# Performance work log

Hardware: AMD Instinct MI355X
Metric: run time of the kernel (lower is better)

Reference implementation:

```python
import jax, jax.numpy as jnp
import numpy as np

D = 1024
HEADS = 16
HD = D // HEADS


def setup_inputs() -> dict:
    key = jax.random.key(0)
    kx, kqkv, kout = jax.random.split(key, 3)
    x = jax.random.normal(kx, (2, 2048, D), dtype=jnp.float32)
    # torch Linear weight is [out, in]; store same layout
    W_qkv = jax.random.normal(kqkv, (3 * D, D), dtype=jnp.float32) * (D ** -0.5)
    W_out = jax.random.normal(kout, (D, D), dtype=jnp.float32) * (D ** -0.5)
    return {"x": x, "W_qkv": W_qkv, "W_out": W_out}


def reference(x, W_qkv, W_out):
    B, T, _ = x.shape
    scale = HD ** -0.5
    qkv = jnp.einsum('btd,ed->bte', x, W_qkv)            # [B,T,3D]
    qkv = qkv.reshape(B, T, 3, HEADS, HD)
    q = jnp.transpose(qkv[:, :, 0], (0, 2, 1, 3))        # [B,H,T,hd]
    k = jnp.transpose(qkv[:, :, 1], (0, 2, 1, 3))
    v = jnp.transpose(qkv[:, :, 2], (0, 2, 1, 3))
    attn = jnp.einsum('bhqd,bhkd->bhqk', q, k) * scale   # [B,H,T,T]
    causal = jnp.tril(jnp.ones((T, T), dtype=bool))
    attn = jnp.where(causal, attn, -jnp.inf)
    attn = jax.nn.softmax(attn, axis=-1)
    out = jnp.einsum('bhqk,bhkd->bhqd', attn, v)         # [B,H,T,hd]
    out = jnp.transpose(out, (0, 2, 1, 3)).reshape(B, T, HEADS * HD)
    return jnp.einsum('btd,ed->bte', out, W_out)
```

## Files before the change

kernel.cpp:

```cpp
#include <hip/hip_runtime.h>
#include <cmath>


typedef unsigned short u16;
typedef unsigned int u32;
typedef short short8 __attribute__((ext_vector_type(8)));
typedef float floatx4 __attribute__((ext_vector_type(4)));

#define T_SZ 2048
#define HD_SZ 64
#define LOG2E 1.44269504088896f

__device__ __forceinline__ u16 f2bf(float f) {
  unsigned u = __float_as_uint(f);
  u += 0x7fffu + ((u >> 16) & 1u);
  return (u16)(u >> 16);
}

__device__ __forceinline__ u32 pack_bf2(float lo, float hi) {
  return __builtin_amdgcn_perm(__float_as_uint(hi), __float_as_uint(lo), 0x07060302u);
}

__device__ __forceinline__ void gload16(const u16* g, u16* l) {
  __builtin_amdgcn_global_load_lds(
      (const __attribute__((address_space(1))) void*)g,
      (__attribute__((address_space(3))) void*)l, 16, 0, 0);
}

__global__ __launch_bounds__(256) void cast3(const float* __restrict__ a, u16* __restrict__ ao, int na4,
                                             const float* __restrict__ b, u16* __restrict__ bo, int nb4,
                                             const float* __restrict__ c, u16* __restrict__ co, int nc4) {
  int i = blockIdx.x * 256 + threadIdx.x;
  const float* src;
  u16* dst;
  int j;
  if (i < na4) { src = a; dst = ao; j = i; }
  else if (i < na4 + nb4) { src = b; dst = bo; j = i - na4; }
  else { j = i - na4 - nb4; if (j >= nc4) return; src = c; dst = co; }
  float4 f = ((const float4*)src)[j];
  ushort4 o;
  o.x = f2bf(f.x); o.y = f2bf(f.y); o.z = f2bf(f.z); o.w = f2bf(f.w);
  ((ushort4*)dst)[j] = o;
}

template <int EPI>
__global__ __launch_bounds__(256) void gemm128(const u16* __restrict__ A,
                                               const u16* __restrict__ Bt,
                                               float* __restrict__ Cout,
                                               u16* __restrict__ Qf,
                                               u16* __restrict__ Kf,
                                               u16* __restrict__ Vf,
                                               int Kdim) {
  __shared__ u16 As[128 * 32];
  __shared__ u16 Bs[128 * 32];
  const int tid = threadIdx.x;
  const int lane = tid & 63;
  const int wave = tid >> 6;
  const int quad = lane >> 4;
  const int l16 = lane & 15;
  const int wm = wave >> 1, wn = wave & 1;
  const int m0 = blockIdx.y * 128;
  const int n0 = blockIdx.x * 128;

  floatx4 acc[4][4];
#pragma unroll
  for (int i = 0; i < 4; i++)
#pragma unroll
    for (int j = 0; j < 4; j++) acc[i][j] = (floatx4){0.f, 0.f, 0.f, 0.f};

  const int lrow = lane >> 2;
  const int pseg = lane & 3;
  const int lseg = pseg ^ ((lane >> 3) & 3);
  const u16* gsrc = (wave < 2) ? A : Bt;
  const int base_rc = (wave < 2) ? m0 : n0;
  u16* lbase = ((wave < 2) ? As : Bs) + ((wave & 1) * 64) * 32;
  const u16* gp[4];
  u16* lp[4];
#pragma unroll
  for (int j = 0; j < 4; j++) {
    const int row = (wave & 1) * 64 + j * 16 + lrow;
    gp[j] = gsrc + (size_t)(base_rc + row) * Kdim + lseg * 8;
    lp[j] = lbase + (j * 16) * 32 + lane * 8;
  }

  const int fsw = ((l16 >> 1) & 3);

  for (int k0 = 0; k0 < Kdim; k0 += 32) {
    __syncthreads();
#pragma unroll
    for (int j = 0; j < 4; j++) gload16(gp[j] + k0, lp[j]);
    __syncthreads();

    short8 af[4], bf[4];
#pragma unroll
    for (int mt = 0; mt < 4; mt++) {
      const int r = wm * 64 + mt * 16 + l16;
      af[mt] = *(const short8*)&As[r * 32 + (quad ^ fsw) * 8];
    }
#pragma unroll
    for (int nt = 0; nt < 4; nt++) {
      const int r = wn * 64 + nt * 16 + l16;
      bf[nt] = *(const short8*)&Bs[r * 32 + (quad ^ fsw) * 8];
    }
#pragma unroll
    for (int mt = 0; mt < 4; mt++)
#pragma unroll
      for (int nt = 0; nt < 4; nt++)
        acc[mt][nt] = __builtin_amdgcn_mfma_f32_16x16x32_bf16(af[mt], bf[nt], acc[mt][nt], 0, 0, 0);
  }

  if constexpr (EPI == 1) {
#pragma unroll
    for (int mt = 0; mt < 4; mt++)
#pragma unroll
      for (int nt = 0; nt < 4; nt++)
#pragma unroll
        for (int r = 0; r < 4; r++) {
          const int m = m0 + wm * 64 + mt * 16 + quad * 4 + r;
          const int n = n0 + wn * 64 + nt * 16 + l16;
          Cout[(size_t)m * 1024 + n] = acc[mt][nt][r];
        }
  } else {
    __shared__ u16 Ep[4][64 * 72];
    u16* ep = &Ep[wave][0];
    const int dest = n0 >> 10;
    const int n0w = n0 + wn * 64;
    const int m_abs = m0 + wm * 64;
    const int b = m_abs >> 11;
    const int t0w = m_abs & 2047;
    const int h = (n0w >> 6) & 15;
    const int bh = b * 16 + h;

    if (dest == 2) {
#pragma unroll
      for (int nt = 0; nt < 4; nt++) {
#pragma unroll
        for (int mt = 0; mt < 4; mt++) {
          uint2 w;
          w.x = pack_bf2(acc[mt][nt][0], acc[mt][nt][1]);
          w.y = pack_bf2(acc[mt][nt][2], acc[mt][nt][3]);
          *(uint2*)&ep[(nt * 16 + l16) * 72 + mt * 16 + quad * 4] = w;
        }
      }
    } else {
      const float sc = (dest == 0) ? 0.125f : 1.0f;
#pragma unroll
      for (int mt = 0; mt < 4; mt++)
#pragma unroll
        for (int nt = 0; nt < 4; nt++)
#pragma unroll
          for (int r = 0; r < 4; r++)
            ep[(mt * 16 + quad * 4 + r) * 72 + nt * 16 + l16] =
                f2bf(acc[mt][nt][r] * sc);
    }

    u16* dstp = (dest == 0) ? Qf : (dest == 1) ? Kf : Vf;
#pragma unroll
    for (int blk = 0; blk < 8; blk++) {
      const int tgd = blk >> 1;
      const int half = blk & 1;
      const int row = tgd * 16 + l16;
      const int col = half * 32 + quad * 8;
      const short8 v = *(const short8*)&ep[row * 72 + col];
      size_t base;
      if (dest == 0)
        base = ((size_t)(bh * 128 + (t0w >> 4) + tgd) * 2 + half) * 512;
      else
        base = (((size_t)(bh * 32 + (t0w >> 6)) * 4 + tgd) * 2 + half) * 512;
      *(short8*)(dstp + base + lane * 8) = v;
    }
  }
}

__global__ __launch_bounds__(256) void flash_attn(const u16* __restrict__ Qf,
                                                  const u16* __restrict__ Kf,
                                                  const u16* __restrict__ Vf,
                                                  u16* __restrict__ Og) {
  __shared__ u16 Ps[4][16 * 72];
  const int tid = threadIdx.x;
  const int lane = tid & 63, wave = tid >> 6;
  const int quad = lane >> 4, l16 = lane & 15;
  const int bh = blockIdx.x, p = blockIdx.y;
  const int b = bh >> 4, h = bh & 15;
  const u16* Qb = Qf + ((size_t)bh << 17);
  const u16* Kb = Kf + ((size_t)bh << 17);
  const u16* Vb = Vf + ((size_t)bh << 17);
  u16* ps = &Ps[wave][0];

  const int gs[2] = {p, 31 - p};

  for (int ph = 0; ph < 2; ph++) {
    const int g = gs[ph];
    const int t0 = g * 64 + wave * 16;
    const u16* qp = Qb + ((size_t)(g * 4 + wave)) * 1024 + lane * 8;
    const short8 qf0 = *(const short8*)qp;
    const short8 qf1 = *(const short8*)(qp + 512);

    float l_sum = 0.f;
    floatx4 o_acc[4];
#pragma unroll
    for (int dt = 0; dt < 4; dt++) o_acc[dt] = (floatx4){0.f, 0.f, 0.f, 0.f};

    for (int kt = 0; kt <= g; kt++) {
      const u16* kp = Kb + (size_t)kt * 4096 + lane * 8;
      const u16* vp = Vb + (size_t)kt * 4096 + lane * 8;
      const bool diag = (kt == g);

      short8 ka[4][2], va[4][2];
#pragma unroll
      for (int nt = 0; nt < 4; nt++) {
        ka[nt][0] = *(const short8*)(kp + (nt * 2 + 0) * 512);
        ka[nt][1] = *(const short8*)(kp + (nt * 2 + 1) * 512);
      }
#pragma unroll
      for (int dt = 0; dt < 4; dt++) {
        va[dt][0] = *(const short8*)(vp + (dt * 2 + 0) * 512);
        va[dt][1] = *(const short8*)(vp + (dt * 2 + 1) * 512);
      }

      floatx4 sacc[4];
#pragma unroll
      for (int nt = 0; nt < 4; nt++) {
        if (diag && nt > wave) continue;
        floatx4 s = (floatx4){0.f, 0.f, 0.f, 0.f};
        s = __builtin_amdgcn_mfma_f32_16x16x32_bf16(ka[nt][0], qf0, s, 0, 0, 0);
        s = __builtin_amdgcn_mfma_f32_16x16x32_bf16(ka[nt][1], qf1, s, 0, 0, 0);
        sacc[nt] = s;
      }

#pragma unroll
      for (int nt = 0; nt < 4; nt++) {
        float p0 = 0.f, p1 = 0.f, p2 = 0.f, p3 = 0.f;
        if (!(diag && nt > wave)) {
          p0 = exp2f(sacc[nt][0] * LOG2E);
          p1 = exp2f(sacc[nt][1] * LOG2E);
          p2 = exp2f(sacc[nt][2] * LOG2E);
          p3 = exp2f(sacc[nt][3] * LOG2E);
          if (diag && nt == wave) {
            if (quad * 4 + 0 > l16) p0 = 0.f;
            if (quad * 4 + 1 > l16) p1 = 0.f;
            if (quad * 4 + 2 > l16) p2 = 0.f;
            if (quad * 4 + 3 > l16) p3 = 0.f;
          }
          l_sum += (p0 + p1) + (p2 + p3);
        }
        uint2 w;
        w.x = pack_bf2(p0, p1);
        w.y = pack_bf2(p2, p3);
        *(uint2*)&ps[l16 * 72 + nt * 16 + quad * 4] = w;
      }

      const short8 pf0 = *(const short8*)&ps[l16 * 72 + quad * 8];
      const short8 pf1 = *(const short8*)&ps[l16 * 72 + 32 + quad * 8];

      const bool skip_hi = diag && (wave < 2);
#pragma unroll
      for (int dt = 0; dt < 4; dt++) {
        o_acc[dt] = __builtin_amdgcn_mfma_f32_16x16x32_bf16(va[dt][0], pf0, o_acc[dt], 0, 0, 0);
        if (!skip_hi)
          o_acc[dt] = __builtin_amdgcn_mfma_f32_16x16x32_bf16(va[dt][1], pf1, o_acc[dt], 0, 0, 0);
      }
    }

    l_sum += __shfl_xor(l_sum, 16, 64);
    l_sum += __shfl_xor(l_sum, 32, 64);
    const float inv_l = 1.0f / l_sum;

    const size_t row = ((size_t)(b * 2048 + t0 + l16) << 10) + h * 64;
#pragma unroll
    for (int dt = 0; dt < 4; dt++) {
      uint2 w;
      w.x = pack_bf2(o_acc[dt][0] * inv_l, o_acc[dt][1] * inv_l);
      w.y = pack_bf2(o_acc[dt][2] * inv_l, o_acc[dt][3] * inv_l);
      *(uint2*)&Og[row + dt * 16 + quad * 4] = w;
    }
  }
}

extern "C" void kernel_launch(void* const* d_in, const int* in_sizes, int n_in,
                              void* d_out, int out_size, void* d_ws, size_t ws_size,
                              hipStream_t stream) {
  const float* x = (const float*)d_in[0];
  const float* Wqkv = (const float*)d_in[1];
  const float* Wout = (const float*)d_in[2];
  float* out = (float*)d_out;

  char* ws = (char*)d_ws;
  u16* xb    = (u16*)(ws + 0);
  u16* wqkvb = (u16*)(ws + 8388608);
  u16* woutb = (u16*)(ws + 14680064);
  u16* Qf    = (u16*)(ws + 16777216);
  u16* Kf    = (u16*)(ws + 25165824);
  u16* Vf    = (u16*)(ws + 33554432);
  u16* attn  = (u16*)(ws + 41943040);

  cast3<<<8192, 256, 0, stream>>>(x, xb, 1048576, Wqkv, wqkvb, 786432,
                                  Wout, woutb, 262144);

  gemm128<0><<<dim3(24, 32), 256, 0, stream>>>(xb, wqkvb, nullptr, Qf, Kf, Vf, 1024);

  flash_attn<<<dim3(32, 16), 256, 0, stream>>>(Qf, Kf, Vf, attn);

  gemm128<1><<<dim3(8, 32), 256, 0, stream>>>(attn, woutb, out, nullptr, nullptr, nullptr, 1024);
}
```

Before: 181.8 us.

## Share K/V loads across paired query tiles and retile output GEMM

Flash attention now processes both paired query tiles in a single K/V loop, loading each K/V tile once and interleaving two independent softmax/PV streams. The log2e factor is folded into the Q scale to drop a multiply per exponent. The output GEMM uses 64-row tiles for more blocks, and the QKV epilogue LDS is halved by staging wave pairs sequentially. This raises register pressure in attention and adds a barrier in the QKV epilogue.

```diff
diff --git a/kernel.cpp b/kernel.cpp
--- a/kernel.cpp
+++ b/kernel.cpp
@@ -9,7 +9,7 @@
 
 #define T_SZ 2048
 #define HD_SZ 64
-#define LOG2E 1.44269504088896f
+#define QSCALE 0.1803368801111244f
 
 __device__ __forceinline__ u16 f2bf(float f) {
   unsigned u = __float_as_uint(f);
@@ -43,16 +43,15 @@
   ((ushort4*)dst)[j] = o;
 }
 
-template <int EPI>
-__global__ __launch_bounds__(256) void gemm128(const u16* __restrict__ A,
-                                               const u16* __restrict__ Bt,
-                                               float* __restrict__ Cout,
-                                               u16* __restrict__ Qf,
-                                               u16* __restrict__ Kf,
-                                               u16* __restrict__ Vf,
-                                               int Kdim) {
+__global__ __launch_bounds__(256) void gemm_qkv(const u16* __restrict__ A,
+                                                const u16* __restrict__ Bt,
+                                                u16* __restrict__ Qf,
+                                                u16* __restrict__ Kf,
+                                                u16* __restrict__ Vf) {
   __shared__ u16 As[128 * 32];
   __shared__ u16 Bs[128 * 32];
+  __shared__ u16 Ep[2][64 * 72];
+  const int Kdim = 1024;
   const int tid = threadIdx.x;
   const int lane = tid & 63;
   const int wave = tid >> 6;
@@ -109,41 +108,29 @@
         acc[mt][nt] = __builtin_amdgcn_mfma_f32_16x16x32_bf16(af[mt], bf[nt], acc[mt][nt], 0, 0, 0);
   }
 
-  if constexpr (EPI == 1) {
-#pragma unroll
-    for (int mt = 0; mt < 4; mt++)
-#pragma unroll
-      for (int nt = 0; nt < 4; nt++)
-#pragma unroll
-        for (int r = 0; r < 4; r++) {
-          const int m = m0 + wm * 64 + mt * 16 + quad * 4 + r;
-          const int n = n0 + wn * 64 + nt * 16 + l16;
-          Cout[(size_t)m * 1024 + n] = acc[mt][nt][r];
-        }
-  } else {
-    __shared__ u16 Ep[4][64 * 72];
-    u16* ep = &Ep[wave][0];
-    const int dest = n0 >> 10;
-    const int n0w = n0 + wn * 64;
-    const int m_abs = m0 + wm * 64;
-    const int b = m_abs >> 11;
-    const int t0w = m_abs & 2047;
-    const int h = (n0w >> 6) & 15;
-    const int bh = b * 16 + h;
-
+  const int dest = n0 >> 10;
+  const int n0w = n0 + wn * 64;
+  const int m_abs = m0 + wm * 64;
+  const int b = m_abs >> 11;
+  const int t0w = m_abs & 2047;
+  const int h = (n0w >> 6) & 15;
+  const int bh = b * 16 + h;
+  u16* dstp = (dest == 0) ? Qf : (dest == 1) ? Kf : Vf;
+
+  auto do_epi = [&](u16* ep) {
     if (dest == 2) {
 #pragma unroll
       for (int nt = 0; nt < 4; nt++) {
 #pragma unroll
         for (int mt = 0; mt < 4; mt++) {
           uint2 w;
-          w.x = pack_bf2(acc[mt][nt][0], acc[mt][nt][1]);
-          w.y = pack_bf2(acc[mt][nt][2], acc[mt][nt][3]);
+          w.x = (u32)f2bf(acc[mt][nt][0]) | ((u32)f2bf(acc[mt][nt][1]) << 16);
+          w.y = (u32)f2bf(acc[mt][nt][2]) | ((u32)f2bf(acc[mt][nt][3]) << 16);
           *(uint2*)&ep[(nt * 16 + l16) * 72 + mt * 16 + quad * 4] = w;
         }
       }
     } else {
-      const float sc = (dest == 0) ? 0.125f : 1.0f;
+      const float sc = (dest == 0) ? QSCALE : 1.0f;
 #pragma unroll
       for (int mt = 0; mt < 4; mt++)
 #pragma unroll
@@ -153,15 +140,11 @@
             ep[(mt * 16 + quad * 4 + r) * 72 + nt * 16 + l16] =
                 f2bf(acc[mt][nt][r] * sc);
     }
-
-    u16* dstp = (dest == 0) ? Qf : (dest == 1) ? Kf : Vf;
 #pragma unroll
     for (int blk = 0; blk < 8; blk++) {
       const int tgd = blk >> 1;
       const int half = blk & 1;
-      const int row = tgd * 16 + l16;
-      const int col = half * 32 + quad * 8;
-      const short8 v = *(const short8*)&ep[row * 72 + col];
+      const short8 v = *(const short8*)&ep[(tgd * 16 + l16) * 72 + half * 32 + quad * 8];
       size_t base;
       if (dest == 0)
         base = ((size_t)(bh * 128 + (t0w >> 4) + tgd) * 2 + half) * 512;
@@ -169,103 +152,191 @@
         base = (((size_t)(bh * 32 + (t0w >> 6)) * 4 + tgd) * 2 + half) * 512;
       *(short8*)(dstp + base + lane * 8) = v;
     }
-  }
+  };
+
+  if (wave < 2) do_epi(&Ep[wave][0]);
+  __syncthreads();
+  if (wave >= 2) do_epi(&Ep[wave - 2][0]);
+}
+
+__global__ __launch_bounds__(256) void gemm_out(const u16* __restrict__ A,
+                                                const u16* __restrict__ Bt,
+                                                float* __restrict__ Cout) {
+  __shared__ u16 As[64 * 32];
+  __shared__ u16 Bs[128 * 32];
+  const int Kdim = 1024;
+  const int tid = threadIdx.x;
+  const int lane = tid & 63;
+  const int wave = tid >> 6;
+  const int quad = lane >> 4;
+  const int l16 = lane & 15;
+  const int wm = wave >> 1, wn = wave & 1;
+  const int m0 = blockIdx.y * 64;
+  const int n0 = blockIdx.x * 128;
+
+  floatx4 acc[2][4];
+#pragma unroll
+  for (int i = 0; i < 2; i++)
+#pragma unroll
+    for (int j = 0; j < 4; j++) acc[i][j] = (floatx4){0.f, 0.f, 0.f, 0.f};
+
+  const int lrow = lane >> 2;
+  const int pseg = lane & 3;
+  const int lseg = pseg ^ ((lane >> 3) & 3);
+  const u16* gp[3];
+  u16* lp[3];
+#pragma unroll
+  for (int j = 0; j < 3; j++) {
+    const int u = wave * 3 + j;
+    if (u < 4) {
+      gp[j] = A + (size_t)(m0 + u * 16 + lrow) * Kdim + lseg * 8;
+      lp[j] = As + u * 512 + lane * 8;
+    } else {
+      const int ub = u - 4;
+      gp[j] = Bt + (size_t)(n0 + ub * 16 + lrow) * Kdim + lseg * 8;
+      lp[j] = Bs + ub * 512 + lane * 8;
+    }
+  }
+
+  const int fsw = ((l16 >> 1) & 3);
+
+  for (int k0 = 0; k0 < Kdim; k0 += 32) {
+    __syncthreads();
+#pragma unroll
+    for (int j = 0; j < 3; j++) gload16(gp[j] + k0, lp[j]);
+    __syncthreads();
+
+    short8 af[2], bf[4];
+#pragma unroll
+    for (int mt = 0; mt < 2; mt++) {
+      const int r = wm * 32 + mt * 16 + l16;
+      af[mt] = *(const short8*)&As[r * 32 + (quad ^ fsw) * 8];
+    }
+#pragma unroll
+    for (int nt = 0; nt < 4; nt++) {
+      const int r = wn * 64 + nt * 16 + l16;
+      bf[nt] = *(const short8*)&Bs[r * 32 + (quad ^ fsw) * 8];
+    }
+#pragma unroll
+    for (int mt = 0; mt < 2; mt++)
+#pragma unroll
+      for (int nt = 0; nt < 4; nt++)
+        acc[mt][nt] = __builtin_amdgcn_mfma_f32_16x16x32_bf16(af[mt], bf[nt], acc[mt][nt], 0, 0, 0);
+  }
+
+#pragma unroll
+  for (int mt = 0; mt < 2; mt++)
+#pragma unroll
+    for (int nt = 0; nt < 4; nt++)
+#pragma unroll
+      for (int r = 0; r < 4; r++) {
+        const int m = m0 + wm * 32 + mt * 16 + quad * 4 + r;
+        const int n = n0 + wn * 64 + nt * 16 + l16;
+        Cout[(size_t)m * 1024 + n] = acc[mt][nt][r];
+      }
 }
 
 __global__ __launch_bounds__(256) void flash_attn(const u16* __restrict__ Qf,
                                                   const u16* __restrict__ Kf,
                                                   const u16* __restrict__ Vf,
                                                   u16* __restrict__ Og) {
-  __shared__ u16 Ps[4][16 * 72];
+  __shared__ u16 Ps[4][2][16 * 72];
   const int tid = threadIdx.x;
   const int lane = tid & 63, wave = tid >> 6;
   const int quad = lane >> 4, l16 = lane & 15;
-  const int bh = blockIdx.x, p = blockIdx.y;
+  const int bh = blockIdx.x;
+  const int py = blockIdx.y;
+  const int p = (py < 8) ? py : 23 - py;
+  const int gA = p, gB = 31 - p;
   const int b = bh >> 4, h = bh & 15;
   const u16* Qb = Qf + ((size_t)bh << 17);
   const u16* Kb = Kf + ((size_t)bh << 17);
   const u16* Vb = Vf + ((size_t)bh << 17);
-  u16* ps = &Ps[wave][0];
-
-  const int gs[2] = {p, 31 - p};
-
-  for (int ph = 0; ph < 2; ph++) {
-    const int g = gs[ph];
-    const int t0 = g * 64 + wave * 16;
-    const u16* qp = Qb + ((size_t)(g * 4 + wave)) * 1024 + lane * 8;
-    const short8 qf0 = *(const short8*)qp;
-    const short8 qf1 = *(const short8*)(qp + 512);
-
-    float l_sum = 0.f;
-    floatx4 o_acc[4];
-#pragma unroll
-    for (int dt = 0; dt < 4; dt++) o_acc[dt] = (floatx4){0.f, 0.f, 0.f, 0.f};
-
-    for (int kt = 0; kt <= g; kt++) {
-      const u16* kp = Kb + (size_t)kt * 4096 + lane * 8;
-      const u16* vp = Vb + (size_t)kt * 4096 + lane * 8;
-      const bool diag = (kt == g);
-
-      short8 ka[4][2], va[4][2];
-#pragma unroll
-      for (int nt = 0; nt < 4; nt++) {
-        ka[nt][0] = *(const short8*)(kp + (nt * 2 + 0) * 512);
-        ka[nt][1] = *(const short8*)(kp + (nt * 2 + 1) * 512);
+
+  const u16* qpA = Qb + ((size_t)(gA * 4 + wave)) * 1024 + lane * 8;
+  const u16* qpB = Qb + ((size_t)(gB * 4 + wave)) * 1024 + lane * 8;
+  const short8 qfA0 = *(const short8*)qpA;
+  const short8 qfA1 = *(const short8*)(qpA + 512);
+  const short8 qfB0 = *(const short8*)qpB;
+  const short8 qfB1 = *(const short8*)(qpB + 512);
+
+  float lA = 0.f, lB = 0.f;
+  floatx4 oA[4], oB[4];
+#pragma unroll
+  for (int dt = 0; dt < 4; dt++) {
+    oA[dt] = (floatx4){0.f, 0.f, 0.f, 0.f};
+    oB[dt] = (floatx4){0.f, 0.f, 0.f, 0.f};
+  }
+  u16* psA = &Ps[wave][0][0];
+  u16* psB = &Ps[wave][1][0];
+
+  short8 ka[4][2], va[4][2];
+
+  auto stream_step = [&](bool diag, const short8& qf0, const short8& qf1,
+                         floatx4* o_acc, float& l_sum, u16* ps) {
+    floatx4 sacc[4];
+#pragma unroll
+    for (int nt = 0; nt < 4; nt++) {
+      if (diag && nt > wave) continue;
+      floatx4 s = (floatx4){0.f, 0.f, 0.f, 0.f};
+      s = __builtin_amdgcn_mfma_f32_16x16x32_bf16(ka[nt][0], qf0, s, 0, 0, 0);
+      s = __builtin_amdgcn_mfma_f32_16x16x32_bf16(ka[nt][1], qf1, s, 0, 0, 0);
+      sacc[nt] = s;
+    }
+#pragma unroll
+    for (int nt = 0; nt < 4; nt++) {
+      float p0 = 0.f, p1 = 0.f, p2 = 0.f, p3 = 0.f;
+      if (!(diag && nt > wave)) {
+        p0 = exp2f(sacc[nt][0]);
+        p1 = exp2f(sacc[nt][1]);
+        p2 = exp2f(sacc[nt][2]);
+        p3 = exp2f(sacc[nt][3]);
+        if (diag && nt == wave) {
+          if (quad * 4 + 0 > l16) p0 = 0.f;
+          if (quad * 4 + 1 > l16) p1 = 0.f;
+          if (quad * 4 + 2 > l16) p2 = 0.f;
+          if (quad * 4 + 3 > l16) p3 = 0.f;
+        }
+        l_sum += (p0 + p1) + (p2 + p3);
       }
-#pragma unroll
-      for (int dt = 0; dt < 4; dt++) {
-        va[dt][0] = *(const short8*)(vp + (dt * 2 + 0) * 512);
-        va[dt][1] = *(const short8*)(vp + (dt * 2 + 1) * 512);
-      }
-
-      floatx4 sacc[4];
-#pragma unroll
-      for (int nt = 0; nt < 4; nt++) {
-        if (diag && nt > wave) continue;
-        floatx4 s = (floatx4){0.f, 0.f, 0.f, 0.f};
-        s = __builtin_amdgcn_mfma_f32_16x16x32_bf16(ka[nt][0], qf0, s, 0, 0, 0);
-        s = __builtin_amdgcn_mfma_f32_16x16x32_bf16(ka[nt][1], qf1, s, 0, 0, 0);
-        sacc[nt] = s;
-      }
-
-#pragma unroll
-      for (int nt = 0; nt < 4; nt++) {
-        float p0 = 0.f, p1 = 0.f, p2 = 0.f, p3 = 0.f;
-        if (!(diag && nt > wave)) {
-          p0 = exp2f(sacc[nt][0] * LOG2E);
-          p1 = exp2f(sacc[nt][1] * LOG2E);
-          p2 = exp2f(sacc[nt][2] * LOG2E);
-          p3 = exp2f(sacc[nt][3] * LOG2E);
-          if (diag && nt == wave) {
-            if (quad * 4 + 0 > l16) p0 = 0.f;
-            if (quad * 4 + 1 > l16) p1 = 0.f;
-            if (quad * 4 + 2 > l16) p2 = 0.f;
-            if (quad * 4 + 3 > l16) p3 = 0.f;
-          }
-          l_sum += (p0 + p1) + (p2 + p3);
-        }
-        uint2 w;
-        w.x = pack_bf2(p0, p1);
-        w.y = pack_bf2(p2, p3);
-        *(uint2*)&ps[l16 * 72 + nt * 16 + quad * 4] = w;
-      }
-
-      const short8 pf0 = *(const short8*)&ps[l16 * 72 + quad * 8];
-      const short8 pf1 = *(const short8*)&ps[l16 * 72 + 32 + quad * 8];
-
-      const bool skip_hi = diag && (wave < 2);
-#pragma unroll
-      for (int dt = 0; dt < 4; dt++) {
-        o_acc[dt] = __builtin_amdgcn_mfma_f32_16x16x32_bf16(va[dt][0], pf0, o_acc[dt], 0, 0, 0);
-        if (!skip_hi)
-          o_acc[dt] = __builtin_amdgcn_mfma_f32_16x16x32_bf16(va[dt][1], pf1, o_acc[dt], 0, 0, 0);
-      }
-    }
-
+      uint2 w;
+      w.x = pack_bf2(p0, p1);
+      w.y = pack_bf2(p2, p3);
+      *(uint2*)&ps[l16 * 72 + nt * 16 + quad * 4] = w;
+    }
+    const short8 pf0 = *(const short8*)&ps[l16 * 72 + quad * 8];
+    const short8 pf1 = *(const short8*)&ps[l16 * 72 + 32 + quad * 8];
+    const bool skip_hi = diag && (wave < 2);
+#pragma unroll
+    for (int dt = 0; dt < 4; dt++) {
+      o_acc[dt] = __builtin_amdgcn_mfma_f32_16x16x32_bf16(va[dt][0], pf0, o_acc[dt], 0, 0, 0);
+      if (!skip_hi)
+        o_acc[dt] = __builtin_amdgcn_mfma_f32_16x16x32_bf16(va[dt][1], pf1, o_acc[dt], 0, 0, 0);
+    }
+  };
+
+  for (int kt = 0; kt <= gB; kt++) {
+    const u16* kp = Kb + (size_t)kt * 4096 + lane * 8;
+    const u16* vp = Vb + (size_t)kt * 4096 + lane * 8;
+#pragma unroll
+    for (int nt = 0; nt < 4; nt++) {
+      ka[nt][0] = *(const short8*)(kp + (nt * 2 + 0) * 512);
+      ka[nt][1] = *(const short8*)(kp + (nt * 2 + 1) * 512);
+    }
+#pragma unroll
+    for (int dt = 0; dt < 4; dt++) {
+      va[dt][0] = *(const short8*)(vp + (dt * 2 + 0) * 512);
+      va[dt][1] = *(const short8*)(vp + (dt * 2 + 1) * 512);
+    }
+    stream_step(kt == gB, qfB0, qfB1, oB, lB, psB);
+    if (kt <= gA) stream_step(kt == gA, qfA0, qfA1, oA, lA, psA);
+  }
+
+  auto write_tile = [&](int g, floatx4* o_acc, float l_sum) {
     l_sum += __shfl_xor(l_sum, 16, 64);
     l_sum += __shfl_xor(l_sum, 32, 64);
     const float inv_l = 1.0f / l_sum;
-
+    const int t0 = g * 64 + wave * 16;
     const size_t row = ((size_t)(b * 2048 + t0 + l16) << 10) + h * 64;
 #pragma unroll
     for (int dt = 0; dt < 4; dt++) {
@@ -274,7 +345,9 @@
       w.y = pack_bf2(o_acc[dt][2] * inv_l, o_acc[dt][3] * inv_l);
       *(uint2*)&Og[row + dt * 16 + quad * 4] = w;
     }
-  }
+  };
+  write_tile(gA, oA, lA);
+  write_tile(gB, oB, lB);
 }
 
 extern "C" void kernel_launch(void* const* d_in, const int* in_sizes, int n_in,
@@ -297,9 +370,9 @@
   cast3<<<8192, 256, 0, stream>>>(x, xb, 1048576, Wqkv, wqkvb, 786432,
                                   Wout, woutb, 262144);
 
-  gemm128<0><<<dim3(24, 32), 256, 0, stream>>>(xb, wqkvb, nullptr, Qf, Kf, Vf, 1024);
+  gemm_qkv<<<dim3(24, 32), 256, 0, stream>>>(xb, wqkvb, Qf, Kf, Vf);
 
   flash_attn<<<dim3(32, 16), 256, 0, stream>>>(Qf, Kf, Vf, attn);
 
-  gemm128<1><<<dim3(8, 32), 256, 0, stream>>>(attn, woutb, out, nullptr, nullptr, nullptr, 1024);
-}
+  gemm_out<<<dim3(8, 64), 256, 0, stream>>>(attn, woutb, out);
+}
```

After: 180.2 us. About the same (-0.9%).
